# Optimization experiments

Hardware: AMD Instinct MI355X
Metric: run time of the kernel (lower is better)

Reference implementation:

```python
import jax, jax.numpy as jnp
import numpy as np

ALPHA_F, GAMMA_F = 0.25, 2.0   # focal loss params
SMOOTH = 1e-6                  # dice smooth
THETA = 5.0                    # boundary weight
W_FOCAL, W_DICE, W_BOUND = 0.3, 0.4, 0.3


def _erode(m):
    # one iteration of scipy binary_erosion, cross (connectivity-1) structure,
    # border_value=0 (outside treated as False)
    p = jnp.pad(m, ((0, 0), (0, 0), (1, 1), (1, 1)), constant_values=False)
    c = p[:, :, 1:-1, 1:-1]
    up = p[:, :, :-2, 1:-1]
    dn = p[:, :, 2:, 1:-1]
    lf = p[:, :, 1:-1, :-2]
    rt = p[:, :, 1:-1, 2:]
    return c & up & dn & lf & rt


def _dilate(m):
    # one iteration of scipy binary_dilation, cross structure, border_value=0
    p = jnp.pad(m, ((0, 0), (0, 0), (1, 1), (1, 1)), constant_values=False)
    c = p[:, :, 1:-1, 1:-1]
    up = p[:, :, :-2, 1:-1]
    dn = p[:, :, 2:, 1:-1]
    lf = p[:, :, 1:-1, :-2]
    rt = p[:, :, 1:-1, 2:]
    return c | up | dn | lf | rt


def setup_inputs() -> dict:
    key = jax.random.key(0)
    k1, k2 = jax.random.split(key)
    B, C, H, W = 64, 1, 512, 512
    inputs = jax.random.normal(k1, (B, C, H, W), dtype=jnp.float32)
    targets = jax.random.randint(k2, (B, C, H, W), 0, 2).astype(jnp.float32)
    return {"inputs": inputs, "targets": targets}


def reference(inputs, targets):
    # numerically stable BCE-with-logits, elementwise
    bce = jnp.maximum(inputs, 0.0) - inputs * targets + jnp.log1p(jnp.exp(-jnp.abs(inputs)))

    # --- focal loss ---
    pt = jnp.exp(-bce)
    focal_loss = jnp.mean(ALPHA_F * (1.0 - pt) ** GAMMA_F * bce)

    # --- dice loss ---
    p = jax.nn.sigmoid(inputs)
    intersection = jnp.sum(p * targets)
    dice = (2.0 * intersection + SMOOTH) / (jnp.sum(p) + jnp.sum(targets) + SMOOTH)
    dice_loss = 1.0 - dice

    # --- boundary-weighted BCE ---
    mask = targets > 0.5
    eroded = _erode(_erode(mask))      # iterations=2
    dilated = _dilate(_dilate(mask))   # iterations=2
    boundary = dilated & (~eroded)
    weights = boundary.astype(jnp.float32) * THETA + 1.0
    boundary_loss = jnp.mean(bce * weights)

    return W_FOCAL * focal_loss + W_DICE * dice_loss + W_BOUND * boundary_loss
```

## Files before the change

kernel.cpp:

```cpp
#include <hip/hip_runtime.h>
#include <math.h>

static constexpr int Hdim = 512;
static constexpr int Wdim = 512;
static constexpr int HW   = Hdim * Wdim;
static constexpr int NIMG = 64;
static constexpr int WPR  = Wdim / 64;
static constexpr int RSTRIP = 32;
static constexpr int SPI  = Hdim / RSTRIP;
static constexpr int NBLK = NIMG * SPI;
static constexpr int MROWS = RSTRIP + 4;
static constexpr int NIT = (RSTRIP * Wdim) / (256 * 4);
static constexpr int WORDS_PER_WAVE = (MROWS * WPR) / 4;


__device__ __forceinline__ unsigned long long shl1(unsigned long long c, unsigned long long l) {
    return (c << 1) | (l >> 63);
}
__device__ __forceinline__ unsigned long long shr1(unsigned long long c, unsigned long long r) {
    return (c >> 1) | (r << 63);
}
__device__ __forceinline__ unsigned long long shl2(unsigned long long c, unsigned long long l) {
    return (c << 2) | (l >> 62);
}
__device__ __forceinline__ unsigned long long shr2(unsigned long long c, unsigned long long r) {
    return (c >> 2) | (r << 62);
}

__global__ __launch_bounds__(256) void combined_loss_kernel(
    const float* __restrict__ inp, const float* __restrict__ tgt,
    float* __restrict__ partials)
{
    __shared__ unsigned long long tmask[MROWS][WPR];
    __shared__ unsigned long long bmask[RSTRIP][WPR];
    __shared__ float smem[4][5];

    const int img   = blockIdx.x / SPI;
    const int strip = blockIdx.x % SPI;
    const int r0    = strip * RSTRIP;
    const float* ib = inp + img * HW;
    const float* tb = tgt + img * HW;

    const int wave = threadIdx.x >> 6;
    const int lane = threadIdx.x & 63;

    unsigned long long* tmflat = &tmask[0][0];
    const int wi_base = wave * WORDS_PER_WAVE;
    #pragma unroll
    for (int g = 0; g < WORDS_PER_WAVE / 4; g++) {
        int wi0 = wi_base + g * 4;
        float v0 = 0.f, v1 = 0.f, v2 = 0.f, v3 = 0.f;
        {
            int gr0 = r0 - 2 + ((wi0 + 0) >> 3);
            int gr1 = r0 - 2 + ((wi0 + 1) >> 3);
            int gr2 = r0 - 2 + ((wi0 + 2) >> 3);
            int gr3 = r0 - 2 + ((wi0 + 3) >> 3);
            if ((unsigned)gr0 < (unsigned)Hdim) v0 = tb[gr0 * Wdim + ((wi0 + 0) & 7) * 64 + lane];
            if ((unsigned)gr1 < (unsigned)Hdim) v1 = tb[gr1 * Wdim + ((wi0 + 1) & 7) * 64 + lane];
            if ((unsigned)gr2 < (unsigned)Hdim) v2 = tb[gr2 * Wdim + ((wi0 + 2) & 7) * 64 + lane];
            if ((unsigned)gr3 < (unsigned)Hdim) v3 = tb[gr3 * Wdim + ((wi0 + 3) & 7) * 64 + lane];
        }
        unsigned long long m0 = __ballot(v0 > 0.5f);
        unsigned long long m1 = __ballot(v1 > 0.5f);
        unsigned long long m2 = __ballot(v2 > 0.5f);
        unsigned long long m3 = __ballot(v3 > 0.5f);
        if (lane == 0) {
            tmflat[wi0 + 0] = m0;
            tmflat[wi0 + 1] = m1;
            tmflat[wi0 + 2] = m2;
            tmflat[wi0 + 3] = m3;
        }
    }
    __syncthreads();

    {
        int row  = threadIdx.x >> 3;
        int word = threadIdx.x & 7;
        int mr = row + 2;

        #define CW(r)  tmask[r][word]
        #define LW(r)  (word > 0 ? tmask[r][word - 1] : 0ULL)
        #define RW(r)  (word < WPR - 1 ? tmask[r][word + 1] : 0ULL)
        unsigned long long c0 = CW(mr),   l0 = LW(mr),   rr0 = RW(mr);
        unsigned long long cm = CW(mr-1), lm = LW(mr-1), rm  = RW(mr-1);
        unsigned long long cp = CW(mr+1), lp = LW(mr+1), rp  = RW(mr+1);
        unsigned long long cm2 = CW(mr-2);
        unsigned long long cp2 = CW(mr+2);
        #undef CW
        #undef LW
        #undef RW

        unsigned long long er =
            c0 & shl1(c0,l0) & shr1(c0,rr0) & shl2(c0,l0) & shr2(c0,rr0)
               & cm & shl1(cm,lm) & shr1(cm,rm)
               & cp & shl1(cp,lp) & shr1(cp,rp)
               & cm2 & cp2;
        unsigned long long di =
            c0 | shl1(c0,l0) | shr1(c0,rr0) | shl2(c0,l0) | shr2(c0,rr0)
               | cm | shl1(cm,lm) | shr1(cm,rm)
               | cp | shl1(cp,lp) | shr1(cp,rp)
               | cm2 | cp2;
        bmask[row][word] = di & ~er;
    }
    __syncthreads();

    float s_focal = 0.f, s_inter = 0.f, s_p = 0.f, s_bw = 0.f;
    int s_tc = 0;

    const float* base = ib + r0 * Wdim + threadIdx.x * 4;
    float4 cur = *(const float4*)(base);
    #pragma unroll
    for (int it = 0; it < NIT; it++) {
        float4 nxt;
        if (it + 1 < NIT) nxt = *(const float4*)(base + (it + 1) * 1024);

        int flat = it * 1024 + threadIdx.x * 4;
        int row  = flat >> 9;
        int x    = flat & (Wdim - 1);
        unsigned int tb4 = (unsigned int)((tmask[row + 2][x >> 6] >> (x & 63)) & 0xFULL);
        unsigned int bb4 = (unsigned int)((bmask[row][x >> 6]     >> (x & 63)) & 0xFULL);
        s_tc += __popc(tb4);
        const float xs[4] = {cur.x, cur.y, cur.z, cur.w};
        #pragma unroll
        for (int k = 0; k < 4; k++) {
            float xi = xs[k];
            bool tpos = (tb4 >> k) & 1;
            float e  = __expf(-fabsf(xi));
            float bce = fmaxf(xi, 0.f) - (tpos ? xi : 0.f) + __logf(1.f + e);
            float rden = __builtin_amdgcn_rcpf(1.f + e);
            float p = (xi >= 0.f ? 1.f : e) * rden;
            float pt = tpos ? p : 1.f - p;
            float om = 1.f - pt;
            s_focal += 0.25f * om * om * bce;
            s_p     += p;
            s_inter += tpos ? p : 0.f;
            float wgt = ((bb4 >> k) & 1) ? 6.0f : 1.0f;
            s_bw += bce * wgt;
        }
        cur = nxt;
    }
    float s_t = (float)s_tc;

    #pragma unroll
    for (int off = 32; off > 0; off >>= 1) {
        s_focal += __shfl_down(s_focal, off);
        s_inter += __shfl_down(s_inter, off);
        s_p     += __shfl_down(s_p,     off);
        s_t     += __shfl_down(s_t,     off);
        s_bw    += __shfl_down(s_bw,    off);
    }
    if (lane == 0) {
        smem[wave][0] = s_focal; smem[wave][1] = s_inter; smem[wave][2] = s_p;
        smem[wave][3] = s_t;     smem[wave][4] = s_bw;
    }
    __syncthreads();
    if (threadIdx.x < 5) {
        float a = smem[0][threadIdx.x] + smem[1][threadIdx.x]
                + smem[2][threadIdx.x] + smem[3][threadIdx.x];
        partials[blockIdx.x * 8 + threadIdx.x] = a;
    }
}

__global__ __launch_bounds__(256) void finalize_kernel(
    const float* __restrict__ partials, float* __restrict__ out)
{
    __shared__ float smem[4][5];
    float a0 = 0.f, a1 = 0.f, a2 = 0.f, a3 = 0.f, a4 = 0.f;
    for (int b = threadIdx.x; b < NBLK; b += 256) {
        const float* s = partials + b * 8;
        a0 += s[0]; a1 += s[1]; a2 += s[2]; a3 += s[3]; a4 += s[4];
    }
    #pragma unroll
    for (int off = 32; off > 0; off >>= 1) {
        a0 += __shfl_down(a0, off);
        a1 += __shfl_down(a1, off);
        a2 += __shfl_down(a2, off);
        a3 += __shfl_down(a3, off);
        a4 += __shfl_down(a4, off);
    }
    int wave = threadIdx.x >> 6;
    int lane = threadIdx.x & 63;
    if (lane == 0) {
        smem[wave][0] = a0; smem[wave][1] = a1; smem[wave][2] = a2;
        smem[wave][3] = a3; smem[wave][4] = a4;
    }
    __syncthreads();
    if (threadIdx.x == 0) {
        double b0 = 0, b1 = 0, b2 = 0, b3 = 0, b4 = 0;
        #pragma unroll
        for (int w = 0; w < 4; w++) {
            b0 += smem[w][0]; b1 += smem[w][1]; b2 += smem[w][2];
            b3 += smem[w][3]; b4 += smem[w][4];
        }
        double invN = 1.0 / (double)(NIMG * HW);
        double focal_loss = b0 * invN;
        double dice = (2.0 * b1 + 1e-6) / (b2 + b3 + 1e-6);
        double boundary_loss = b4 * invN;
        out[0] = (float)(0.3 * focal_loss + 0.4 * (1.0 - dice) + 0.3 * boundary_loss);
    }
}

extern "C" void kernel_launch(void* const* d_in, const int* in_sizes, int n_in,
                              void* d_out, int out_size, void* d_ws, size_t ws_size,
                              hipStream_t stream) {
    const float* inp = (const float*)d_in[0];
    const float* tgt = (const float*)d_in[1];
    float* out = (float*)d_out;
    float* partials = (float*)d_ws;

    combined_loss_kernel<<<NBLK, 256, 0, stream>>>(inp, tgt, partials);
    finalize_kernel<<<1, 256, 0, stream>>>(partials, out);
}
```

Measured before the change: 174.8 us.

## Split mask/boundary computation into separate kernel with bitmask buffer

```diff
diff --git a/kernel.cpp b/kernel.cpp
--- a/kernel.cpp
+++ b/kernel.cpp
@@ -6,12 +6,17 @@
 static constexpr int HW   = Hdim * Wdim;
 static constexpr int NIMG = 64;
 static constexpr int WPR  = Wdim / 64;
-static constexpr int RSTRIP = 32;
+static constexpr int WPI  = Hdim * WPR;
+static constexpr int RSTRIP = 16;
 static constexpr int SPI  = Hdim / RSTRIP;
-static constexpr int NBLK = NIMG * SPI;
+static constexpr int NBLK_M = NIMG * SPI;
 static constexpr int MROWS = RSTRIP + 4;
-static constexpr int NIT = (RSTRIP * Wdim) / (256 * 4);
-static constexpr int WORDS_PER_WAVE = (MROWS * WPR) / 4;
+static constexpr int MWORDS = MROWS * WPR;
+static constexpr int WPW = MWORDS / 4;
+static constexpr int NBLK_C = 2048;
+static constexpr int CTHREADS = NBLK_C * 256;
+static constexpr int F4TOTAL = NIMG * HW / 4;
+static constexpr int CITERS = F4TOTAL / CTHREADS;
 
 
 __device__ __forceinline__ unsigned long long shl1(unsigned long long c, unsigned long long l) {
@@ -27,39 +32,32 @@
     return (c >> 2) | (r << 62);
 }
 
-__global__ __launch_bounds__(256) void combined_loss_kernel(
-    const float* __restrict__ inp, const float* __restrict__ tgt,
-    float* __restrict__ partials)
+__global__ __launch_bounds__(256) void maskbound_kernel(
+    const float* __restrict__ tgt, ulonglong2* __restrict__ comb)
 {
     __shared__ unsigned long long tmask[MROWS][WPR];
-    __shared__ unsigned long long bmask[RSTRIP][WPR];
-    __shared__ float smem[4][5];
 
     const int img   = blockIdx.x / SPI;
     const int strip = blockIdx.x % SPI;
     const int r0    = strip * RSTRIP;
-    const float* ib = inp + img * HW;
     const float* tb = tgt + img * HW;
 
     const int wave = threadIdx.x >> 6;
     const int lane = threadIdx.x & 63;
 
     unsigned long long* tmflat = &tmask[0][0];
-    const int wi_base = wave * WORDS_PER_WAVE;
-    #pragma unroll
-    for (int g = 0; g < WORDS_PER_WAVE / 4; g++) {
-        int wi0 = wi_base + g * 4;
+    #pragma unroll
+    for (int g = 0; g < WPW / 4; g++) {
+        int wi0 = wave * WPW + g * 4;
         float v0 = 0.f, v1 = 0.f, v2 = 0.f, v3 = 0.f;
-        {
-            int gr0 = r0 - 2 + ((wi0 + 0) >> 3);
-            int gr1 = r0 - 2 + ((wi0 + 1) >> 3);
-            int gr2 = r0 - 2 + ((wi0 + 2) >> 3);
-            int gr3 = r0 - 2 + ((wi0 + 3) >> 3);
-            if ((unsigned)gr0 < (unsigned)Hdim) v0 = tb[gr0 * Wdim + ((wi0 + 0) & 7) * 64 + lane];
-            if ((unsigned)gr1 < (unsigned)Hdim) v1 = tb[gr1 * Wdim + ((wi0 + 1) & 7) * 64 + lane];
-            if ((unsigned)gr2 < (unsigned)Hdim) v2 = tb[gr2 * Wdim + ((wi0 + 2) & 7) * 64 + lane];
-            if ((unsigned)gr3 < (unsigned)Hdim) v3 = tb[gr3 * Wdim + ((wi0 + 3) & 7) * 64 + lane];
-        }
+        int gr0 = r0 - 2 + ((wi0 + 0) >> 3);
+        int gr1 = r0 - 2 + ((wi0 + 1) >> 3);
+        int gr2 = r0 - 2 + ((wi0 + 2) >> 3);
+        int gr3 = r0 - 2 + ((wi0 + 3) >> 3);
+        if ((unsigned)gr0 < (unsigned)Hdim) v0 = tb[gr0 * Wdim + ((wi0 + 0) & 7) * 64 + lane];
+        if ((unsigned)gr1 < (unsigned)Hdim) v1 = tb[gr1 * Wdim + ((wi0 + 1) & 7) * 64 + lane];
+        if ((unsigned)gr2 < (unsigned)Hdim) v2 = tb[gr2 * Wdim + ((wi0 + 2) & 7) * 64 + lane];
+        if ((unsigned)gr3 < (unsigned)Hdim) v3 = tb[gr3 * Wdim + ((wi0 + 3) & 7) * 64 + lane];
         unsigned long long m0 = __ballot(v0 > 0.5f);
         unsigned long long m1 = __ballot(v1 > 0.5f);
         unsigned long long m2 = __ballot(v2 > 0.5f);
@@ -73,7 +71,7 @@
     }
     __syncthreads();
 
-    {
+    if (threadIdx.x < RSTRIP * WPR) {
         int row  = threadIdx.x >> 3;
         int word = threadIdx.x & 7;
         int mr = row + 2;
@@ -100,27 +98,33 @@
                | cm | shl1(cm,lm) | shr1(cm,rm)
                | cp | shl1(cp,lp) | shr1(cp,rp)
                | cm2 | cp2;
-        bmask[row][word] = di & ~er;
-    }
-    __syncthreads();
-
+
+        ulonglong2 pair;
+        pair.x = c0;
+        pair.y = di & ~er;
+        comb[img * WPI + (r0 + row) * WPR + word] = pair;
+    }
+}
+
+__global__ __launch_bounds__(256, 4) void combined_loss_kernel(
+    const float* __restrict__ inp, const ulonglong2* __restrict__ comb,
+    float* __restrict__ partials)
+{
+    const int tid = blockIdx.x * 256 + threadIdx.x;
     float s_focal = 0.f, s_inter = 0.f, s_p = 0.f, s_bw = 0.f;
     int s_tc = 0;
 
-    const float* base = ib + r0 * Wdim + threadIdx.x * 4;
-    float4 cur = *(const float4*)(base);
-    #pragma unroll
-    for (int it = 0; it < NIT; it++) {
-        float4 nxt;
-        if (it + 1 < NIT) nxt = *(const float4*)(base + (it + 1) * 1024);
-
-        int flat = it * 1024 + threadIdx.x * 4;
-        int row  = flat >> 9;
-        int x    = flat & (Wdim - 1);
-        unsigned int tb4 = (unsigned int)((tmask[row + 2][x >> 6] >> (x & 63)) & 0xFULL);
-        unsigned int bb4 = (unsigned int)((bmask[row][x >> 6]     >> (x & 63)) & 0xFULL);
+    #pragma unroll
+    for (int it = 0; it < CITERS; it++) {
+        const int f4 = tid + it * CTHREADS;
+        const float4 v = ((const float4*)inp)[f4];
+        const int wi = f4 >> 4;
+        const int sh = (f4 & 15) * 4;
+        const ulonglong2 cb = comb[wi];
+        unsigned int tb4 = (unsigned int)((cb.x >> sh) & 0xFULL);
+        unsigned int bb4 = (unsigned int)((cb.y >> sh) & 0xFULL);
         s_tc += __popc(tb4);
-        const float xs[4] = {cur.x, cur.y, cur.z, cur.w};
+        const float xs[4] = {v.x, v.y, v.z, v.w};
         #pragma unroll
         for (int k = 0; k < 4; k++) {
             float xi = xs[k];
@@ -137,10 +141,12 @@
             float wgt = ((bb4 >> k) & 1) ? 6.0f : 1.0f;
             s_bw += bce * wgt;
         }
-        cur = nxt;
     }
     float s_t = (float)s_tc;
 
+    __shared__ float smem[4][5];
+    const int wave = threadIdx.x >> 6;
+    const int lane = threadIdx.x & 63;
     #pragma unroll
     for (int off = 32; off > 0; off >>= 1) {
         s_focal += __shfl_down(s_focal, off);
@@ -166,7 +172,7 @@
 {
     __shared__ float smem[4][5];
     float a0 = 0.f, a1 = 0.f, a2 = 0.f, a3 = 0.f, a4 = 0.f;
-    for (int b = threadIdx.x; b < NBLK; b += 256) {
+    for (int b = threadIdx.x; b < NBLK_C; b += 256) {
         const float* s = partials + b * 8;
         a0 += s[0]; a1 += s[1]; a2 += s[2]; a3 += s[3]; a4 += s[4];
     }
@@ -206,8 +212,11 @@
     const float* inp = (const float*)d_in[0];
     const float* tgt = (const float*)d_in[1];
     float* out = (float*)d_out;
-    float* partials = (float*)d_ws;
-
-    combined_loss_kernel<<<NBLK, 256, 0, stream>>>(inp, tgt, partials);
+    char* ws = (char*)d_ws;
+    float* partials = (float*)ws;
+    ulonglong2* comb = (ulonglong2*)(ws + (4u << 20));
+
+    maskbound_kernel<<<NBLK_M, 256, 0, stream>>>(tgt, comb);
+    combined_loss_kernel<<<NBLK_C, 256, 0, stream>>>(inp, comb, partials);
     finalize_kernel<<<1, 256, 0, stream>>>(partials, out);
 }
```

New measurement: 164.8 us. 1.06x faster.
